# Kernel optimization log

Hardware: AMD Instinct MI355X
Metric: run time of the kernel (lower is better)

Reference implementation:

```python
import jax, jax.numpy as jnp
import numpy as np

# ---------- e3nn-style machinery, max_l = 1, real basis ----------
_EPS3 = np.zeros((3, 3, 3), dtype=np.float64)
_EPS3[0, 1, 2] = _EPS3[1, 2, 0] = _EPS3[2, 0, 1] = 1.0
_EPS3[0, 2, 1] = _EPS3[2, 1, 0] = _EPS3[1, 0, 2] = -1.0
W3J = {
    (0, 0, 0): np.ones((1, 1, 1)),
    (0, 1, 1): np.eye(3)[None, :, :] / np.sqrt(3.0),
    (1, 0, 1): np.eye(3)[:, None, :] / np.sqrt(3.0),
    (1, 1, 0): np.eye(3)[:, :, None] / np.sqrt(3.0),
    (1, 1, 1): _EPS3 / np.sqrt(6.0),
}

# irreps as (mul, l, parity)
IR_SH    = [(1, 0, 1), (1, 1, -1)]                      # 1x0e+1x1o (dim 4)
IR_INTER = [(4, 0, 1), (4, 0, -1), (2, 1, -1), (2, 1, 1)]  # gate.irreps_in (dim 20)
IR_GOUT  = [(2, 0, 1), (2, 0, -1), (2, 1, -1), (2, 1, 1)]  # gate.irreps_out (dim 16)
IR_OUT   = [(1, 1, -1), (1, 1, 1)]                      # 1x1o+1x1e (dim 6)

def _offsets(ir):
    off, o = [], 0
    for m, l, _ in ir:
        off.append(o)
        o += m * (2 * l + 1)
    return off, o

def build_tp(ir1, ir2, iro):
    """Fully-connected TP instructions: component irrep-norm, element path-norm."""
    fan = [0.0] * len(iro)
    paths = []
    for io, (mo, lo, po) in enumerate(iro):
        for i1, (m1, l1, p1) in enumerate(ir1):
            for i2, (m2, l2, p2) in enumerate(ir2):
                if p1 * p2 == po and abs(l1 - l2) <= lo <= l1 + l2:
                    paths.append((i1, i2, io))
                    fan[io] += m1 * m2
    ins, woff = [], 0
    for i1, i2, io in paths:
        m1, l1, _ = ir1[i1]; m2, l2, _ = ir2[i2]; mo, lo, _ = iro[io]
        alpha = float(np.sqrt((2 * lo + 1) / fan[io]))
        ins.append((i1, i2, io, alpha, woff))
        woff += m1 * m2 * mo
    return ins, woff

INS1, NUMEL1 = build_tp(IR_SH, IR_SH, IR_INTER)   # weight_numel = 14
INS2, NUMEL2 = build_tp(IR_GOUT, IR_SH, IR_OUT)   # weight_numel = 12

def tp_apply(ir1, ir2, iro, ins, x1, x2, w):
    off1, _ = _offsets(ir1); off2, _ = _offsets(ir2); offo, _ = _offsets(iro)
    lead = x1.shape[:-1]
    out = [None] * len(iro)
    for i1, i2, io, alpha, woff in ins:
        m1, l1, _ = ir1[i1]; m2, l2, _ = ir2[i2]; mo, lo, _ = iro[io]
        x1b = x1[..., off1[i1]:off1[i1] + m1 * (2 * l1 + 1)].reshape(lead + (m1, 2 * l1 + 1))
        x2b = x2[..., off2[i2]:off2[i2] + m2 * (2 * l2 + 1)].reshape(lead + (m2, 2 * l2 + 1))
        wb = w[..., woff:woff + m1 * m2 * mo].reshape(lead + (m1, m2, mo))
        C = jnp.asarray(W3J[(l1, l2, lo)], dtype=x1.dtype)
        blk = alpha * jnp.einsum('...ui,...vj,ijk,...uvw->...wk', x1b, x2b, C, wb)
        out[io] = blk if out[io] is None else out[io] + blk
    pieces = []
    for io, (mo, lo, _) in enumerate(iro):
        b = out[io] if out[io] is not None else jnp.zeros(lead + (mo, 2 * lo + 1), x1.dtype)
        pieces.append(b.reshape(lead + (mo * (2 * lo + 1),)))
    return jnp.concatenate(pieces, axis=-1)

def fc_net(x, w1, w2):
    # e3nn FullyConnectedNet: h = relu(x @ W1 / sqrt(fan_in)) * sqrt(2); out = h @ W2 / sqrt(fan)
    h = jax.nn.relu(x @ w1 / np.sqrt(w1.shape[0])) * np.sqrt(2.0)
    return h @ w2 / np.sqrt(w2.shape[0])

def gate_fn(x):
    # input irreps: [4x0e | 4x0o | 2x1o | 2x1e]; within 0e: 2 scalars + gates g1,g3; within 0o: 2 scalars + gates g2,g4
    lead = x.shape[:-1]
    se = jax.nn.relu(x[..., 0:2])
    ge = x[..., 2:4]
    so = jnp.abs(x[..., 4:6])
    go = x[..., 6:8]
    v1o = x[..., 8:14].reshape(lead + (2, 3))
    v1e = x[..., 14:20].reshape(lead + (2, 3))
    g1 = jax.nn.relu(ge[..., 0:1]); g3 = jax.nn.relu(ge[..., 1:2])
    g2 = jnp.tanh(go[..., 0:1]);    g4 = jnp.tanh(go[..., 1:2])
    v1o_out = jnp.concatenate([v1o[..., 0, :] * g1, v1o[..., 1, :] * g2], axis=-1)
    v1e_out = jnp.concatenate([v1e[..., 0, :] * g3, v1e[..., 1, :] * g4], axis=-1)
    return jnp.concatenate([se, so, v1o_out, v1e_out], axis=-1)  # [..., 16]

def sph_l1(d):
    # spherical harmonics l<=1, normalize=True, normalization='component' (e3nn l=1 order: y,z,x)
    n = jnp.sqrt(jnp.sum(d * d, axis=-1, keepdims=True) + 1e-12)
    u = d / n
    ones = jnp.ones(d.shape[:-1] + (1,), d.dtype)
    return jnp.concatenate([ones, np.sqrt(3.0) * u[..., [1, 2, 0]]], axis=-1)  # [..., 4]

def global_conv(ir1, iro, ins, nf, edge_attr, atten, normalizer, w1, w2):
    w = fc_net(atten, w1, w2)                                   # [B,N,N,numel]
    B, N = nf.shape[0], nf.shape[1]
    nfe = jnp.broadcast_to(nf[:, None, :, :], (B, N, N, nf.shape[-1]))  # node j at edge (i,j)
    ef = tp_apply(ir1, IR_SH, iro, ins, nfe, edge_attr, w)      # [B,N,N,dim_out]
    return jnp.sum(ef, axis=1) / normalizer

def _forward(attn_disp, attn_mask, coordinates, fc1_w1, fc1_w2, fc2_w1, fc2_w2):
    B, H, N, _ = attn_disp.shape
    normalizer = jnp.sqrt(jnp.sum((~jnp.isinf(attn_disp[:, 0])).astype(coordinates.dtype), axis=-1))[..., None]  # [B,N,1]
    ad = jnp.transpose(attn_disp, (0, 2, 3, 1))                 # [B,N,N,H]
    ad = jnp.where(jnp.isinf(ad), jnp.zeros((), ad.dtype), ad)
    # unit displacement (zero on diagonal)
    d = coordinates[:, :, None, :] - coordinates[:, None, :, :]
    d = d / (jnp.sqrt(jnp.sum(d * d, axis=-1, keepdims=True) + 1e-12) + 1e-5)
    edge_features = sph_l1(d)                                   # [B,N,N,4]
    nf = jnp.sum(edge_features, axis=1) / normalizer            # [B,N,4]
    nf = global_conv(IR_SH, IR_INTER, INS1, nf, edge_features, ad, normalizer, fc1_w1, fc1_w2)   # [B,N,20]
    nf = gate_fn(nf)                                            # [B,N,16]
    nf = global_conv(IR_GOUT, IR_OUT, INS2, nf, edge_features, ad, normalizer, fc2_w1, fc2_w2)   # [B,N,6]
    return ad, attn_mask, coordinates, nf, edge_features

def setup_inputs() -> dict:
    key = jax.random.key(0)
    ks = jax.random.split(key, 8)
    B, H, N = 4, 16, 512
    return {
        'attn_disp': jax.random.normal(ks[0], (B, H, N, N), jnp.float32),
        'attn_mask': jax.random.normal(ks[1], (B * H, N, N), jnp.float32),
        'coordinates': jax.random.normal(ks[2], (B, N, 3), jnp.float32),
        'fc1_w1': jax.random.normal(ks[3], (H, 2 * H), jnp.float32),
        'fc1_w2': jax.random.normal(ks[4], (2 * H, NUMEL1), jnp.float32),
        'fc2_w1': jax.random.normal(ks[5], (H, 2 * H), jnp.float32),
        'fc2_w2': jax.random.normal(ks[6], (2 * H, NUMEL2), jnp.float32),
    }

def reference(attn_disp, attn_mask, coordinates, fc1_w1, fc1_w2, fc2_w1, fc2_w2):
    return _forward(attn_disp, attn_mask, coordinates, fc1_w1, fc1_w2, fc2_w1, fc2_w2)
```

## Files before the change

### kernel.cpp

```cpp
#include <hip/hip_runtime.h>
#include <cmath>

#define NN 512

__device__ __forceinline__ int is_inf_f(float x) {
    return (__float_as_uint(x) & 0x7fffffffu) == 0x7f800000u;
}

__device__ __forceinline__ void edge_vec(float ci0, float ci1, float ci2,
                                         float cj0, float cj1, float cj2,
                                         float& e0, float& e1, float& e2) {
    float d0 = ci0 - cj0, d1 = ci1 - cj1, d2 = ci2 - cj2;
    float den = sqrtf(d0*d0 + d1*d1 + d2*d2 + 1e-12f) + 1e-5f;
    float r = 1.0f / den;
    d0 *= r; d1 *= r; d2 *= r;
    float n = sqrtf(d0*d0 + d1*d1 + d2*d2 + 1e-12f);
    float s = 1.7320508075688772f / n;
    e0 = d1 * s;
    e1 = d2 * s;
    e2 = d0 * s;
}

__global__ __launch_bounds__(256) void k_stage(
    const float* __restrict__ disp, const float* __restrict__ mask,
    const float* __restrict__ coords,
    float* __restrict__ ad_out, float* __restrict__ mask_out,
    float* __restrict__ coords_out, float* __restrict__ ef_out,
    float* __restrict__ ws_norm)
{
    const int blk = blockIdx.x;
    const int b = blk >> 9, i = blk & 511;
    const int tid = threadIdx.x;
    const float ci0 = coords[(b*NN+i)*3+0];
    const float ci1 = coords[(b*NN+i)*3+1];
    const float ci2 = coords[(b*NN+i)*3+2];
    int cnt = 0;
    #pragma unroll
    for (int r = 0; r < 2; r++) {
        const int j = r*256 + tid;
        float v[16];
        #pragma unroll
        for (int h = 0; h < 16; h++) {
            float x = disp[((b*16+h)*NN + i)*NN + j];
            int bad = is_inf_f(x);
            if (h == 0) cnt += 1 - bad;
            v[h] = bad ? 0.0f : x;
        }
        float4* dst = (float4*)(ad_out + (size_t)((b*NN+i)*NN + j)*16);
        dst[0] = make_float4(v[0], v[1], v[2], v[3]);
        dst[1] = make_float4(v[4], v[5], v[6], v[7]);
        dst[2] = make_float4(v[8], v[9], v[10], v[11]);
        dst[3] = make_float4(v[12], v[13], v[14], v[15]);
        const float cj0 = coords[(b*NN+j)*3+0];
        const float cj1 = coords[(b*NN+j)*3+1];
        const float cj2 = coords[(b*NN+j)*3+2];
        float e0, e1, e2;
        edge_vec(ci0, ci1, ci2, cj0, cj1, cj2, e0, e1, e2);
        ((float4*)ef_out)[(b*NN+i)*NN + j] = make_float4(1.0f, e0, e1, e2);
    }
    {
        const float4* mi = (const float4*)mask;
        float4* mo = (float4*)mask_out;
        const int mbase = blk * 2048;
        #pragma unroll
        for (int r = 0; r < 8; r++) mo[mbase + r*256 + tid] = mi[mbase + r*256 + tid];
    }
    if (blk == 0) {
        for (int idx = tid; idx < 4*NN*3; idx += 256) coords_out[idx] = coords[idx];
    }
    #pragma unroll
    for (int off = 32; off >= 1; off >>= 1) cnt += __shfl_down(cnt, off);
    __shared__ int sred[4];
    if ((tid & 63) == 0) sred[tid >> 6] = cnt;
    __syncthreads();
    if (tid == 0) ws_norm[blk] = sqrtf((float)(sred[0]+sred[1]+sred[2]+sred[3]));
}

__global__ __launch_bounds__(256) void k_reduce(
    const float* __restrict__ ad, const float* __restrict__ coords,
    const float* __restrict__ wA, const float* __restrict__ wB,
    float* __restrict__ ws)
{
    __shared__ float W0[512], W1[512];
    __shared__ float A[256*17];
    __shared__ float E[256*3];
    __shared__ float sred[12];
    const int blk = blockIdx.x;
    const int b = blk >> 9, j = blk & 511;
    const int tid = threadIdx.x;
    const int i_slot = tid & 31, c_slot = tid >> 5, c0 = c_slot * 4;
    W0[tid] = wA[tid]; W0[tid+256] = wA[tid+256];
    W1[tid] = wB[tid]; W1[tid+256] = wB[tid+256];
    const float cj0 = coords[(b*NN+j)*3+0];
    const float cj1 = coords[(b*NN+j)*3+1];
    const float cj2 = coords[(b*NN+j)*3+2];
    float se0 = 0.f, se1 = 0.f, se2 = 0.f;
    float acc[2][4][4];
    #pragma unroll
    for (int n = 0; n < 2; n++)
        #pragma unroll
        for (int c = 0; c < 4; c++)
            #pragma unroll
            for (int w = 0; w < 4; w++) acc[n][c][w] = 0.f;

    for (int s = 0; s < 2; s++) {
        __syncthreads();
        const int i = s*256 + tid;
        const float4* src = (const float4*)(ad + (size_t)((b*NN+i)*NN + j)*16);
        float4 v0 = src[0], v1 = src[1], v2 = src[2], v3 = src[3];
        const int ab = tid*17;
        A[ab+ 0]=v0.x; A[ab+ 1]=v0.y; A[ab+ 2]=v0.z; A[ab+ 3]=v0.w;
        A[ab+ 4]=v1.x; A[ab+ 5]=v1.y; A[ab+ 6]=v1.z; A[ab+ 7]=v1.w;
        A[ab+ 8]=v2.x; A[ab+ 9]=v2.y; A[ab+10]=v2.z; A[ab+11]=v2.w;
        A[ab+12]=v3.x; A[ab+13]=v3.y; A[ab+14]=v3.z; A[ab+15]=v3.w;
        const float ci0 = coords[(b*NN+i)*3+0];
        const float ci1 = coords[(b*NN+i)*3+1];
        const float ci2 = coords[(b*NN+i)*3+2];
        float e0, e1, e2;
        edge_vec(ci0, ci1, ci2, cj0, cj1, cj2, e0, e1, e2);
        E[tid*3+0]=e0; E[tid*3+1]=e1; E[tid*3+2]=e2;
        se0 += e0; se1 += e1; se2 += e2;
        __syncthreads();
        for (int half = 0; half < 2; half++) {
            float a[4][16], ee[4][3];
            #pragma unroll
            for (int q = 0; q < 4; q++) {
                const int il = i_slot + 32*(half*4+q);
                const int ba = il*17;
                #pragma unroll
                for (int h = 0; h < 16; h++) a[q][h] = A[ba+h];
                ee[q][0]=E[il*3+0]; ee[q][1]=E[il*3+1]; ee[q][2]=E[il*3+2];
            }
            #pragma unroll
            for (int c = 0; c < 4; c++) {
                const int cc = c0 + c;
                #pragma unroll
                for (int net = 0; net < 2; net++) {
                    const float* __restrict__ Wn = net ? W1 : W0;
                    float t[4] = {0.f, 0.f, 0.f, 0.f};
                    #pragma unroll
                    for (int h = 0; h < 16; h++) {
                        const float w = Wn[h*32+cc];
                        #pragma unroll
                        for (int q = 0; q < 4; q++) t[q] = fmaf(a[q][h], w, t[q]);
                    }
                    #pragma unroll
                    for (int q = 0; q < 4; q++) {
                        const float hq = fmaxf(t[q]*0.25f, 0.f) * 1.4142135623730951f;
                        acc[net][c][0] += hq;
                        acc[net][c][1] = fmaf(ee[q][0], hq, acc[net][c][1]);
                        acc[net][c][2] = fmaf(ee[q][1], hq, acc[net][c][2]);
                        acc[net][c][3] = fmaf(ee[q][2], hq, acc[net][c][3]);
                    }
                }
            }
        }
    }
    #pragma unroll
    for (int n = 0; n < 2; n++)
        #pragma unroll
        for (int c = 0; c < 4; c++)
            #pragma unroll
            for (int w = 0; w < 4; w++) {
                float v = acc[n][c][w];
                v += __shfl_xor(v, 1); v += __shfl_xor(v, 2); v += __shfl_xor(v, 4);
                v += __shfl_xor(v, 8); v += __shfl_xor(v, 16);
                acc[n][c][w] = v;
            }
    if (i_slot == 0) {
        float* accg = ws + 2048*4 + (size_t)blk*256;
        #pragma unroll
        for (int n = 0; n < 2; n++)
            #pragma unroll
            for (int w = 0; w < 4; w++)
                #pragma unroll
                for (int c = 0; c < 4; c++)
                    accg[(n*4+w)*32 + c0 + c] = acc[n][c][w];
    }
    #pragma unroll
    for (int off = 1; off < 64; off <<= 1) {
        se0 += __shfl_xor(se0, off);
        se1 += __shfl_xor(se1, off);
        se2 += __shfl_xor(se2, off);
    }
    if ((tid & 63) == 0) {
        const int wv = tid >> 6;
        sred[wv*3+0] = se0; sred[wv*3+1] = se1; sred[wv*3+2] = se2;
    }
    __syncthreads();
    if (tid == 0) {
        float* seg = ws + 2048 + blk*3;
        seg[0] = sred[0]+sred[3]+sred[6]+sred[9];
        seg[1] = sred[1]+sred[4]+sred[7]+sred[10];
        seg[2] = sred[2]+sred[5]+sred[8]+sred[11];
    }
}

__global__ __launch_bounds__(256) void k_final(
    const float* __restrict__ ws,
    const float* __restrict__ w2a,
    const float* __restrict__ w2b,
    float* __restrict__ nf_out)
{
    const int bj = blockIdx.x*256 + threadIdx.x;
    const float inv = 1.0f / ws[bj];
    const float s  = 512.0f * inv;
    const float vv0 = ws[2048 + bj*3 + 0] * inv;
    const float vv1 = ws[2048 + bj*3 + 1] * inv;
    const float vv2 = ws[2048 + bj*3 + 2] * inv;
    const float* acc = ws + 2048*4 + (size_t)bj*256;
    const float ksc = 0.17677669529663687f;
    float S0[14], S1[3][14];
    #pragma unroll
    for (int cc = 0; cc < 14; cc++) { S0[cc]=0.f; S1[0][cc]=0.f; S1[1][cc]=0.f; S1[2][cc]=0.f; }
    for (int c = 0; c < 32; c++) {
        const float p = acc[c], q0 = acc[32+c], q1 = acc[64+c], q2 = acc[96+c];
        #pragma unroll
        for (int cc = 0; cc < 14; cc++) {
            const float w = w2a[c*14+cc];
            S0[cc]    = fmaf(p,  w, S0[cc]);
            S1[0][cc] = fmaf(q0, w, S1[0][cc]);
            S1[1][cc] = fmaf(q1, w, S1[1][cc]);
            S1[2][cc] = fmaf(q2, w, S1[2][cc]);
        }
    }
    #pragma unroll
    for (int cc = 0; cc < 14; cc++) { S0[cc]*=ksc; S1[0][cc]*=ksc; S1[1][cc]*=ksc; S1[2][cc]*=ksc; }
    const float is2 = 0.7071067811865476f;
    const float is3 = 0.5773502691896258f;
    float x0[4];
    #pragma unroll
    for (int k = 0; k < 4; k++)
        x0[k] = inv*is2*( s*S0[k] + is3*(vv0*S1[0][4+k] + vv1*S1[1][4+k] + vv2*S1[2][4+k]) );
    const float vv[3] = {vv0, vv1, vv2};
    float x8[3];
    #pragma unroll
    for (int k = 0; k < 3; k++)
        x8[k] = inv*is2*( s*S1[k][8] + vv[k]*S0[10] );
    const float E12_0=S1[0][12], E12_1=S1[1][12], E12_2=S1[2][12];
    float x14[3];
    x14[0] = inv*is2*(vv1*E12_2 - vv2*E12_1);
    x14[1] = inv*is2*(vv2*E12_0 - vv0*E12_2);
    x14[2] = inv*is2*(vv0*E12_1 - vv1*E12_0);
    const float a0 = fmaxf(x0[0],0.f), a1 = fmaxf(x0[1],0.f);
    const float g1 = fmaxf(x0[2],0.f), g3 = fmaxf(x0[3],0.f);
    const float p0=x8[0]*g1,  p1=x8[1]*g1,  p2=x8[2]*g1;
    const float q0_=x14[0]*g3, q1_=x14[1]*g3, q2_=x14[2]*g3;
    float T0[12], T1[3][12];
    #pragma unroll
    for (int cc = 0; cc < 12; cc++){ T0[cc]=0.f; T1[0][cc]=0.f; T1[1][cc]=0.f; T1[2][cc]=0.f; }
    const float* acc2 = acc + 128;
    for (int c = 0; c < 32; c++) {
        const float p = acc2[c], r0 = acc2[32+c], r1 = acc2[64+c], r2 = acc2[96+c];
        #pragma unroll
        for (int cc = 0; cc < 12; cc++) {
            const float w = w2b[c*12+cc];
            T0[cc]    = fmaf(p,  w, T0[cc]);
            T1[0][cc] = fmaf(r0, w, T1[0][cc]);
            T1[1][cc] = fmaf(r1, w, T1[1][cc]);
            T1[2][cc] = fmaf(r2, w, T1[2][cc]);
        }
    }
    #pragma unroll
    for (int cc = 0; cc < 12; cc++){ T0[cc]*=ksc; T1[0][cc]*=ksc; T1[1][cc]*=ksc; T1[2][cc]*=ksc; }
    const float is6  = 0.4082482904638631f;
    const float is12 = 0.28867513459481287f;
    const float E0[3] = {T1[0][0], T1[1][0], T1[2][0]};
    const float E1[3] = {T1[0][1], T1[1][1], T1[2][1]};
    const float E4[3] = {T1[0][4], T1[1][4], T1[2][4]};
    const float E8[3] = {T1[0][8], T1[1][8], T1[2][8]};
    const float cq0 = q1_*E4[2] - q2_*E4[1];
    const float cq1 = q2_*E4[0] - q0_*E4[2];
    const float cq2 = q0_*E4[1] - q1_*E4[0];
    const float cp0 = p1*E8[2] - p2*E8[1];
    const float cp1 = p2*E8[0] - p0*E8[2];
    const float cp2 = p0*E8[1] - p1*E8[0];
    float o[6];
    o[0] = inv*( is6*(a0*E0[0] + a1*E1[0]) + is6*p0*T0[2] + is12*cq0 );
    o[1] = inv*( is6*(a0*E0[1] + a1*E1[1]) + is6*p1*T0[2] + is12*cq1 );
    o[2] = inv*( is6*(a0*E0[2] + a1*E1[2]) + is6*p2*T0[2] + is12*cq2 );
    o[3] = inv*( is12*cp0 + is6*q0_*T0[10] );
    o[4] = inv*( is12*cp1 + is6*q1_*T0[10] );
    o[5] = inv*( is12*cp2 + is6*q2_*T0[10] );
    #pragma unroll
    for (int k = 0; k < 6; k++) nf_out[bj*6+k] = o[k];
}

extern "C" void kernel_launch(void* const* d_in, const int* in_sizes, int n_in,
                              void* d_out, int out_size, void* d_ws, size_t ws_size,
                              hipStream_t stream) {
    const float* disp   = (const float*)d_in[0];
    const float* mask   = (const float*)d_in[1];
    const float* coords = (const float*)d_in[2];
    const float* fc1w1  = (const float*)d_in[3];
    const float* fc1w2  = (const float*)d_in[4];
    const float* fc2w1  = (const float*)d_in[5];
    const float* fc2w2  = (const float*)d_in[6];
    float* out = (float*)d_out;
    float* ad_out     = out;
    float* mask_out   = out + 16777216;
    float* coords_out = out + 33554432;
    float* nf_out     = coords_out + 6144;
    float* ef_out     = nf_out + 12288;
    float* ws = (float*)d_ws;

    k_stage <<<2048, 256, 0, stream>>>(disp, mask, coords, ad_out, mask_out,
                                       coords_out, ef_out, ws);
    k_reduce<<<2048, 256, 0, stream>>>(ad_out, coords, fc1w1, fc2w1, ws);
    k_final <<<8,    256, 0, stream>>>(ws, fc1w2, fc2w2, nf_out);
}
```

Baseline: 374.6 us.

## Split reduce over i-chunks, load rows directly to registers, LDS-based final reduction

k_reduce now splits each (b,j) column's 512 i-rows into NCHUNK chunks across separate blocks, doubling the grid to 4096 when workspace allows. Each thread loads its ad rows straight into registers instead of staging through shared memory, which removes the per-iteration syncs. The cross-lane shuffle reduction is replaced by a shared-memory transpose and sum, and the partial sums are combined later in k_final, now launched as 32 blocks of 64 threads. The aim is more parallelism and fewer barriers in the dominant reduce kernel. The cost is uncoalesced per-thread strided loads and extra workspace traffic.

```diff
diff --git a/kernel.cpp b/kernel.cpp
--- a/kernel.cpp
+++ b/kernel.cpp
@@ -76,21 +76,26 @@
     if (tid == 0) ws_norm[blk] = sqrtf((float)(sred[0]+sred[1]+sred[2]+sred[3]));
 }
 
-__global__ __launch_bounds__(256) void k_reduce(
+template<int NCHUNK>
+__global__ __launch_bounds__(256, 4) void k_reduce(
     const float* __restrict__ ad, const float* __restrict__ coords,
     const float* __restrict__ wA, const float* __restrict__ wB,
     float* __restrict__ ws)
 {
-    __shared__ float W0[512], W1[512];
-    __shared__ float A[256*17];
-    __shared__ float E[256*3];
-    __shared__ float sred[12];
+    constexpr int CH = NN / NCHUNK;
+    constexpr int Q  = CH / 32;
+    constexpr size_t SE_OFF  = 2048;
+    constexpr size_t ACC_OFF = 2048 + (size_t)2048*NCHUNK*3;
+    __shared__ float W[1024];
+    __shared__ float R[256*20];
     const int blk = blockIdx.x;
-    const int b = blk >> 9, j = blk & 511;
+    const int bj = blk / NCHUNK, chunk = blk % NCHUNK;
+    const int b = bj >> 9, j = bj & 511;
     const int tid = threadIdx.x;
     const int i_slot = tid & 31, c_slot = tid >> 5, c0 = c_slot * 4;
-    W0[tid] = wA[tid]; W0[tid+256] = wA[tid+256];
-    W1[tid] = wB[tid]; W1[tid+256] = wB[tid+256];
+    W[tid]     = wA[tid]; W[tid+256] = wA[tid+256];
+    W[tid+512] = wB[tid]; W[tid+768] = wB[tid+256];
+    __syncthreads();
     const float cj0 = coords[(b*NN+j)*3+0];
     const float cj1 = coords[(b*NN+j)*3+1];
     const float cj2 = coords[(b*NN+j)*3+2];
@@ -103,118 +108,113 @@
             #pragma unroll
             for (int w = 0; w < 4; w++) acc[n][c][w] = 0.f;
 
-    for (int s = 0; s < 2; s++) {
-        __syncthreads();
-        const int i = s*256 + tid;
-        const float4* src = (const float4*)(ad + (size_t)((b*NN+i)*NN + j)*16);
-        float4 v0 = src[0], v1 = src[1], v2 = src[2], v3 = src[3];
-        const int ab = tid*17;
-        A[ab+ 0]=v0.x; A[ab+ 1]=v0.y; A[ab+ 2]=v0.z; A[ab+ 3]=v0.w;
-        A[ab+ 4]=v1.x; A[ab+ 5]=v1.y; A[ab+ 6]=v1.z; A[ab+ 7]=v1.w;
-        A[ab+ 8]=v2.x; A[ab+ 9]=v2.y; A[ab+10]=v2.z; A[ab+11]=v2.w;
-        A[ab+12]=v3.x; A[ab+13]=v3.y; A[ab+14]=v3.z; A[ab+15]=v3.w;
-        const float ci0 = coords[(b*NN+i)*3+0];
-        const float ci1 = coords[(b*NN+i)*3+1];
-        const float ci2 = coords[(b*NN+i)*3+2];
-        float e0, e1, e2;
-        edge_vec(ci0, ci1, ci2, cj0, cj1, cj2, e0, e1, e2);
-        E[tid*3+0]=e0; E[tid*3+1]=e1; E[tid*3+2]=e2;
-        se0 += e0; se1 += e1; se2 += e2;
-        __syncthreads();
-        for (int half = 0; half < 2; half++) {
-            float a[4][16], ee[4][3];
-            #pragma unroll
-            for (int q = 0; q < 4; q++) {
-                const int il = i_slot + 32*(half*4+q);
-                const int ba = il*17;
-                #pragma unroll
-                for (int h = 0; h < 16; h++) a[q][h] = A[ba+h];
-                ee[q][0]=E[il*3+0]; ee[q][1]=E[il*3+1]; ee[q][2]=E[il*3+2];
-            }
+    #pragma unroll
+    for (int g = 0; g < Q/4; g++) {
+        float a[4][16], ee[4][3];
+        #pragma unroll
+        for (int u = 0; u < 4; u++) {
+            const int q = g*4 + u;
+            const int i = chunk*CH + q*32 + i_slot;
+            const float4* src = (const float4*)(ad + (size_t)((b*NN+i)*NN + j)*16);
+            float4 v0 = src[0], v1 = src[1], v2 = src[2], v3 = src[3];
+            a[u][0]=v0.x; a[u][1]=v0.y; a[u][2]=v0.z; a[u][3]=v0.w;
+            a[u][4]=v1.x; a[u][5]=v1.y; a[u][6]=v1.z; a[u][7]=v1.w;
+            a[u][8]=v2.x; a[u][9]=v2.y; a[u][10]=v2.z; a[u][11]=v2.w;
+            a[u][12]=v3.x; a[u][13]=v3.y; a[u][14]=v3.z; a[u][15]=v3.w;
+            const float ci0 = coords[(b*NN+i)*3+0];
+            const float ci1 = coords[(b*NN+i)*3+1];
+            const float ci2 = coords[(b*NN+i)*3+2];
+            edge_vec(ci0, ci1, ci2, cj0, cj1, cj2, ee[u][0], ee[u][1], ee[u][2]);
+            if (c_slot == 0) { se0 += ee[u][0]; se1 += ee[u][1]; se2 += ee[u][2]; }
+        }
+        #pragma unroll
+        for (int net = 0; net < 2; net++) {
             #pragma unroll
             for (int c = 0; c < 4; c++) {
-                const int cc = c0 + c;
+                float t[4] = {0.f, 0.f, 0.f, 0.f};
+                const float* __restrict__ Wn = &W[net*512 + c0 + c];
                 #pragma unroll
-                for (int net = 0; net < 2; net++) {
-                    const float* __restrict__ Wn = net ? W1 : W0;
-                    float t[4] = {0.f, 0.f, 0.f, 0.f};
+                for (int h = 0; h < 16; h++) {
+                    const float wv = Wn[h*32];
                     #pragma unroll
-                    for (int h = 0; h < 16; h++) {
-                        const float w = Wn[h*32+cc];
-                        #pragma unroll
-                        for (int q = 0; q < 4; q++) t[q] = fmaf(a[q][h], w, t[q]);
-                    }
-                    #pragma unroll
-                    for (int q = 0; q < 4; q++) {
-                        const float hq = fmaxf(t[q]*0.25f, 0.f) * 1.4142135623730951f;
-                        acc[net][c][0] += hq;
-                        acc[net][c][1] = fmaf(ee[q][0], hq, acc[net][c][1]);
-                        acc[net][c][2] = fmaf(ee[q][1], hq, acc[net][c][2]);
-                        acc[net][c][3] = fmaf(ee[q][2], hq, acc[net][c][3]);
-                    }
+                    for (int u = 0; u < 4; u++) t[u] = fmaf(a[u][h], wv, t[u]);
+                }
+                #pragma unroll
+                for (int u = 0; u < 4; u++) {
+                    const float hq = fmaxf(t[u]*0.25f, 0.f) * 1.4142135623730951f;
+                    acc[net][c][0] += hq;
+                    acc[net][c][1] = fmaf(ee[u][0], hq, acc[net][c][1]);
+                    acc[net][c][2] = fmaf(ee[u][1], hq, acc[net][c][2]);
+                    acc[net][c][3] = fmaf(ee[u][2], hq, acc[net][c][3]);
                 }
             }
         }
     }
-    #pragma unroll
-    for (int n = 0; n < 2; n++)
-        #pragma unroll
-        for (int c = 0; c < 4; c++)
+    if (tid < 32) {
+        #pragma unroll
+        for (int off = 1; off < 32; off <<= 1) {
+            se0 += __shfl_xor(se0, off);
+            se1 += __shfl_xor(se1, off);
+            se2 += __shfl_xor(se2, off);
+        }
+        if (tid == 0) {
+            float* seg = ws + SE_OFF + (size_t)(bj*NCHUNK + chunk)*3;
+            seg[0] = se0; seg[1] = se1; seg[2] = se2;
+        }
+    }
+    float* accg = ws + ACC_OFF + (size_t)(bj*NCHUNK + chunk)*256;
+    #pragma unroll
+    for (int net = 0; net < 2; net++) {
+        __syncthreads();
+        #pragma unroll
+        for (int w = 0; w < 4; w++)
+            *(float4*)(&R[tid*20 + w*4]) =
+                make_float4(acc[net][0][w], acc[net][1][w], acc[net][2][w], acc[net][3][w]);
+        __syncthreads();
+        if (tid < 128) {
+            const int w = tid >> 5, c = tid & 31, cs = c >> 2, cl = c & 3;
+            const int v = w*4 + cl;
+            float s = 0.f;
             #pragma unroll
-            for (int w = 0; w < 4; w++) {
-                float v = acc[n][c][w];
-                v += __shfl_xor(v, 1); v += __shfl_xor(v, 2); v += __shfl_xor(v, 4);
-                v += __shfl_xor(v, 8); v += __shfl_xor(v, 16);
-                acc[n][c][w] = v;
-            }
-    if (i_slot == 0) {
-        float* accg = ws + 2048*4 + (size_t)blk*256;
-        #pragma unroll
-        for (int n = 0; n < 2; n++)
-            #pragma unroll
-            for (int w = 0; w < 4; w++)
-                #pragma unroll
-                for (int c = 0; c < 4; c++)
-                    accg[(n*4+w)*32 + c0 + c] = acc[n][c][w];
-    }
-    #pragma unroll
-    for (int off = 1; off < 64; off <<= 1) {
-        se0 += __shfl_xor(se0, off);
-        se1 += __shfl_xor(se1, off);
-        se2 += __shfl_xor(se2, off);
-    }
-    if ((tid & 63) == 0) {
-        const int wv = tid >> 6;
-        sred[wv*3+0] = se0; sred[wv*3+1] = se1; sred[wv*3+2] = se2;
-    }
-    __syncthreads();
-    if (tid == 0) {
-        float* seg = ws + 2048 + blk*3;
-        seg[0] = sred[0]+sred[3]+sred[6]+sred[9];
-        seg[1] = sred[1]+sred[4]+sred[7]+sred[10];
-        seg[2] = sred[2]+sred[5]+sred[8]+sred[11];
-    }
-}
-
-__global__ __launch_bounds__(256) void k_final(
+            for (int l = 0; l < 32; l++) s += R[(cs*32 + l)*20 + v];
+            accg[net*128 + w*32 + c] = s;
+        }
+    }
+}
+
+template<int NCHUNK>
+__global__ __launch_bounds__(64) void k_final(
     const float* __restrict__ ws,
     const float* __restrict__ w2a,
     const float* __restrict__ w2b,
     float* __restrict__ nf_out)
 {
-    const int bj = blockIdx.x*256 + threadIdx.x;
+    constexpr size_t SE_OFF  = 2048;
+    constexpr size_t ACC_OFF = 2048 + (size_t)2048*NCHUNK*3;
+    const int bj = blockIdx.x*64 + threadIdx.x;
     const float inv = 1.0f / ws[bj];
     const float s  = 512.0f * inv;
-    const float vv0 = ws[2048 + bj*3 + 0] * inv;
-    const float vv1 = ws[2048 + bj*3 + 1] * inv;
-    const float vv2 = ws[2048 + bj*3 + 2] * inv;
-    const float* acc = ws + 2048*4 + (size_t)bj*256;
+    float sse[3] = {0.f, 0.f, 0.f};
+    #pragma unroll
+    for (int ch = 0; ch < NCHUNK; ch++) {
+        sse[0] += ws[SE_OFF + (size_t)(bj*NCHUNK+ch)*3 + 0];
+        sse[1] += ws[SE_OFF + (size_t)(bj*NCHUNK+ch)*3 + 1];
+        sse[2] += ws[SE_OFF + (size_t)(bj*NCHUNK+ch)*3 + 2];
+    }
+    const float vv0 = sse[0] * inv, vv1 = sse[1] * inv, vv2 = sse[2] * inv;
+    const float* accb = ws + ACC_OFF + (size_t)bj*NCHUNK*256;
     const float ksc = 0.17677669529663687f;
     float S0[14], S1[3][14];
     #pragma unroll
     for (int cc = 0; cc < 14; cc++) { S0[cc]=0.f; S1[0][cc]=0.f; S1[1][cc]=0.f; S1[2][cc]=0.f; }
+    #pragma unroll 4
     for (int c = 0; c < 32; c++) {
-        const float p = acc[c], q0 = acc[32+c], q1 = acc[64+c], q2 = acc[96+c];
+        float p = 0.f, q0 = 0.f, q1 = 0.f, q2 = 0.f;
+        #pragma unroll
+        for (int ch = 0; ch < NCHUNK; ch++) {
+            const float* a = accb + ch*256;
+            p += a[c]; q0 += a[32+c]; q1 += a[64+c]; q2 += a[96+c];
+        }
         #pragma unroll
         for (int cc = 0; cc < 14; cc++) {
             const float w = w2a[c*14+cc];
@@ -249,9 +249,14 @@
     float T0[12], T1[3][12];
     #pragma unroll
     for (int cc = 0; cc < 12; cc++){ T0[cc]=0.f; T1[0][cc]=0.f; T1[1][cc]=0.f; T1[2][cc]=0.f; }
-    const float* acc2 = acc + 128;
+    #pragma unroll 4
     for (int c = 0; c < 32; c++) {
-        const float p = acc2[c], r0 = acc2[32+c], r1 = acc2[64+c], r2 = acc2[96+c];
+        float p = 0.f, r0 = 0.f, r1 = 0.f, r2 = 0.f;
+        #pragma unroll
+        for (int ch = 0; ch < NCHUNK; ch++) {
+            const float* a = accb + ch*256 + 128;
+            p += a[c]; r0 += a[32+c]; r1 += a[64+c]; r2 += a[96+c];
+        }
         #pragma unroll
         for (int cc = 0; cc < 12; cc++) {
             const float w = w2b[c*12+cc];
@@ -304,8 +309,13 @@
     float* ef_out     = nf_out + 12288;
     float* ws = (float*)d_ws;
 
-    k_stage <<<2048, 256, 0, stream>>>(disp, mask, coords, ad_out, mask_out,
-                                       coords_out, ef_out, ws);
-    k_reduce<<<2048, 256, 0, stream>>>(ad_out, coords, fc1w1, fc2w1, ws);
-    k_final <<<8,    256, 0, stream>>>(ws, fc1w2, fc2w2, nf_out);
-}
+    k_stage<<<2048, 256, 0, stream>>>(disp, mask, coords, ad_out, mask_out,
+                                      coords_out, ef_out, ws);
+    if (ws_size >= (size_t)5*1024*1024) {
+        k_reduce<2><<<4096, 256, 0, stream>>>(ad_out, coords, fc1w1, fc2w1, ws);
+        k_final<2><<<32, 64, 0, stream>>>(ws, fc1w2, fc2w2, nf_out);
+    } else {
+        k_reduce<1><<<2048, 256, 0, stream>>>(ad_out, coords, fc1w1, fc2w1, ws);
+        k_final<1><<<32, 64, 0, stream>>>(ws, fc1w2, fc2w2, nf_out);
+    }
+}
```

Measured after the change: 710.9 us. 89.8% more time.
